# Optimization experiments

Hardware: AMD Instinct MI355X
Metric: run time of the kernel (lower is better)

## Reference

```python
import jax, jax.numpy as jnp
import numpy as np

B, N, T, C = 2, 2048, 32, 32
NUM_BASES, MAX_K, K_CURR = 4, 32, 16


def setup_inputs() -> dict:
    key = jax.random.key(0)
    k1, k2, k3, k4, k5 = jax.random.split(key, 5)
    z = jax.random.normal(k1, (B, N, T, C), dtype=jnp.float32)
    neighbor_indices = jax.random.randint(k2, (N, K_CURR), 0, N)
    # parameters (match torch init scales)
    adjacency = 0.5 + 0.01 * jax.random.normal(k3, (N, MAX_K), dtype=jnp.float32)
    basis_weights = 0.02 * jax.random.normal(k4, (NUM_BASES, N, MAX_K), dtype=jnp.float32)
    channel_coeffs = jax.random.normal(k5, (C, NUM_BASES), dtype=jnp.float32)
    return {
        "z": z,
        "neighbor_indices": neighbor_indices,
        "adjacency": adjacency,
        "basis_weights": basis_weights,
        "channel_coeffs": channel_coeffs,
    }


def reference(z, neighbor_indices, adjacency, basis_weights, channel_coeffs):
    # z: [B,N,T,C], neighbor_indices: [N,k]
    k = neighbor_indices.shape[1]
    bases = basis_weights[:, :, :k]        # [num_bases, N, k]
    adj = adjacency[:, :k]                 # [N, k]
    # per-channel effective edge weights: [C, N, k]
    eff = jnp.einsum('cb,bnk->cnk', channel_coeffs, bases)
    edge_w = eff * adj[None, :, :]         # [C, N, k]
    w = jnp.transpose(edge_w, (1, 2, 0))   # [N, k, C]
    # gather neighbor features: [B, N, k, T, C]
    z_neigh = z[:, neighbor_indices]
    # weighted sum over neighbors, per-channel weights
    out = jnp.einsum('bnktc,nkc->bntc', z_neigh, w)
    return jnp.tanh(out)
```

## Files before the change

### kernel.cpp

```cpp
#include <hip/hip_runtime.h>


constexpr int BB_    = 2;
constexpr int NN_    = 2048;
constexpr int TT_    = 32;
constexpr int CC_    = 32;
constexpr int NBASE_ = 4;
constexpr int MAXK_  = 32;
constexpr int KC_    = 16;

__device__ __forceinline__ float fast_tanh(float x) {
    float e = __expf(2.0f * x);
    float r = __builtin_amdgcn_rcpf(e + 1.0f);
    return fmaf(-2.0f, r, 1.0f);
}

__global__ __launch_bounds__(256) void cgl_kernel(
    const float* __restrict__ z,
    const int*   __restrict__ nbr,
    const float* __restrict__ adj,
    const float* __restrict__ bw,
    const float* __restrict__ cc,
    float*       __restrict__ out)
{
    __shared__ __align__(16) float w_s[KC_][CC_];
    __shared__ float bw_s[NBASE_][KC_];
    __shared__ float cc_s[CC_ * NBASE_];
    __shared__ float adj_s[KC_];
    __shared__ int   idx_s[KC_];

    const int tid = threadIdx.x;
    const int blk = blockIdx.x;
    const int b   = blk >> 11;
    const int n   = blk & (NN_ - 1);

    if (tid < NBASE_ * KC_) {
        int bb = tid >> 4, k = tid & 15;
        bw_s[bb][k] = bw[((size_t)bb * NN_ + n) * MAXK_ + k];
    } else if (tid >= 64 && tid < 64 + CC_ * NBASE_) {
        int i = tid - 64;
        cc_s[i] = cc[i];
    } else if (tid >= 192 && tid < 192 + KC_) {
        int k = tid - 192;
        adj_s[k] = adj[(size_t)n * MAXK_ + k];
        idx_s[k] = nbr[n * KC_ + k];
    }
    __syncthreads();

    {
        int i = tid;
        #pragma unroll
        for (int r = 0; r < 2; ++r, i += 256) {
            int k = i >> 5, c = i & 31;
            float s = cc_s[c * NBASE_ + 0] * bw_s[0][k]
                    + cc_s[c * NBASE_ + 1] * bw_s[1][k]
                    + cc_s[c * NBASE_ + 2] * bw_s[2][k]
                    + cc_s[c * NBASE_ + 3] * bw_s[3][k];
            w_s[k][c] = s * adj_s[k];
        }
    }
    __syncthreads();

    const int c0 = (tid << 2) & 31;
    const float4* __restrict__ z4 = (const float4*)z;
    const size_t zb = (size_t)b * NN_ * (TT_ * CC_ / 4);

    float4 acc = make_float4(0.f, 0.f, 0.f, 0.f);
    #pragma unroll
    for (int k = 0; k < KC_; ++k) {
        const int nk = idx_s[k];
        float4 zv = z4[zb + (size_t)nk * (TT_ * CC_ / 4) + tid];
        float4 wv = *(const float4*)&w_s[k][c0];
        acc.x = fmaf(zv.x, wv.x, acc.x);
        acc.y = fmaf(zv.y, wv.y, acc.y);
        acc.z = fmaf(zv.z, wv.z, acc.z);
        acc.w = fmaf(zv.w, wv.w, acc.w);
    }

    float4 o;
    o.x = fast_tanh(acc.x);
    o.y = fast_tanh(acc.y);
    o.z = fast_tanh(acc.z);
    o.w = fast_tanh(acc.w);
    ((float4*)out)[(size_t)blk * 256 + tid] = o;
}

extern "C" void kernel_launch(void* const* d_in, const int* in_sizes, int n_in,
                              void* d_out, int out_size, void* d_ws, size_t ws_size,
                              hipStream_t stream) {
    const float* z   = (const float*)d_in[0];
    const int*   nbr = (const int*)d_in[1];
    const float* adj = (const float*)d_in[2];
    const float* bw  = (const float*)d_in[3];
    const float* cc  = (const float*)d_in[4];
    float* out = (float*)d_out;

    cgl_kernel<<<dim3(BB_ * NN_), dim3(256), 0, stream>>>(z, nbr, adj, bw, cc, out);
}
```

Measured before the change: 96.64 us.

## Stage z slices in LDS per (b,t,channel-quarter) and precompute bf16 edge weights

Splits the work into a prep kernel that computes the per-channel edge weights once and stores them as packed bf16 in workspace, plus a main kernel that loads a full (batch, time, 8-channel) slice of z for all nodes into LDS. Neighbor gathers then read LDS instead of scattered global memory, and the duplicated per-block weight computation is removed. This adds a second launch and a large shared-memory footprint per block. Rounding the weights to bf16 lowers their precision.

Result: slower. 104.9 us (+8.5%).

```diff
diff --git a/kernel.cpp b/kernel.cpp
--- a/kernel.cpp
+++ b/kernel.cpp
@@ -15,74 +15,114 @@
     return fmaf(-2.0f, r, 1.0f);
 }
 
-__global__ __launch_bounds__(256) void cgl_kernel(
-    const float* __restrict__ z,
-    const int*   __restrict__ nbr,
+__device__ __forceinline__ unsigned pack_bf16(float x, float y) {
+    unsigned ux = __float_as_uint(x), uy = __float_as_uint(y);
+    ux = (ux + 0x7fffu + ((ux >> 16) & 1u)) >> 16;
+    uy = (uy + 0x7fffu + ((uy >> 16) & 1u)) >> 16;
+    return ux | (uy << 16);
+}
+__device__ __forceinline__ float blo(unsigned u) { return __uint_as_float(u << 16); }
+__device__ __forceinline__ float bhi(unsigned u) { return __uint_as_float(u & 0xffff0000u); }
+
+__global__ __launch_bounds__(512) void prep_w(
     const float* __restrict__ adj,
     const float* __restrict__ bw,
     const float* __restrict__ cc,
+    uint4*       __restrict__ w16)
+{
+    const int gid = blockIdx.x * 512 + threadIdx.x;
+    const int n = gid >> 4, k = gid & 15;
+
+    const float a  = adj[n * MAXK_ + k];
+    const float b0 = bw[(0 * NN_ + n) * MAXK_ + k];
+    const float b1 = bw[(1 * NN_ + n) * MAXK_ + k];
+    const float b2 = bw[(2 * NN_ + n) * MAXK_ + k];
+    const float b3 = bw[(3 * NN_ + n) * MAXK_ + k];
+
+    #pragma unroll
+    for (int cq = 0; cq < 4; ++cq) {
+        unsigned u[4];
+        #pragma unroll
+        for (int j = 0; j < 4; ++j) {
+            int c0 = cq * 8 + 2 * j;
+            float w0 = a * (cc[c0 * 4 + 0] * b0 + cc[c0 * 4 + 1] * b1 +
+                            cc[c0 * 4 + 2] * b2 + cc[c0 * 4 + 3] * b3);
+            float w1 = a * (cc[(c0 + 1) * 4 + 0] * b0 + cc[(c0 + 1) * 4 + 1] * b1 +
+                            cc[(c0 + 1) * 4 + 2] * b2 + cc[(c0 + 1) * 4 + 3] * b3);
+            u[j] = pack_bf16(w0, w1);
+        }
+        w16[((size_t)cq * NN_ + n) * KC_ + k] = make_uint4(u[0], u[1], u[2], u[3]);
+    }
+}
+
+__global__ __launch_bounds__(512, 4) void cgl_main(
+    const float* __restrict__ z,
+    const int*   __restrict__ nbr,
+    const uint4* __restrict__ w16,
     float*       __restrict__ out)
 {
-    __shared__ __align__(16) float w_s[KC_][CC_];
-    __shared__ float bw_s[NBASE_][KC_];
-    __shared__ float cc_s[CC_ * NBASE_];
-    __shared__ float adj_s[KC_];
-    __shared__ int   idx_s[KC_];
+    __shared__ float4 zl0[NN_];
+    __shared__ float4 zl1[NN_];
 
-    const int tid = threadIdx.x;
-    const int blk = blockIdx.x;
-    const int b   = blk >> 11;
-    const int n   = blk & (NN_ - 1);
+    const int tid   = threadIdx.x;
+    const int g     = blockIdx.x;
+    const int bt    = g & 63;
+    const int inner = g >> 6;
+    const int cq    = inner >> 1;
+    const int s     = inner & 1;
+    const int b     = bt >> 5;
+    const int t     = bt & 31;
 
-    if (tid < NBASE_ * KC_) {
-        int bb = tid >> 4, k = tid & 15;
-        bw_s[bb][k] = bw[((size_t)bb * NN_ + n) * MAXK_ + k];
-    } else if (tid >= 64 && tid < 64 + CC_ * NBASE_) {
-        int i = tid - 64;
-        cc_s[i] = cc[i];
-    } else if (tid >= 192 && tid < 192 + KC_) {
-        int k = tid - 192;
-        adj_s[k] = adj[(size_t)n * MAXK_ + k];
-        idx_s[k] = nbr[n * KC_ + k];
+    const float* zbase = z + ((size_t)b * NN_ * TT_ + t) * CC_ + cq * 8;
+    #pragma unroll
+    for (int r = 0; r < 4; ++r) {
+        int n = r * 512 + tid;
+        const float4* p = (const float4*)(zbase + (size_t)n * (TT_ * CC_));
+        zl0[n] = p[0];
+        zl1[n] = p[1];
     }
     __syncthreads();
 
-    {
-        int i = tid;
+    #pragma unroll
+    for (int r = 0; r < 2; ++r) {
+        const int n = s * 1024 + r * 512 + tid;
+
+        const int4* ip = (const int4*)(nbr + n * KC_);
+        int4 i0 = ip[0], i1 = ip[1], i2 = ip[2], i3 = ip[3];
+        int idxs[16] = { i0.x, i0.y, i0.z, i0.w,  i1.x, i1.y, i1.z, i1.w,
+                         i2.x, i2.y, i2.z, i2.w,  i3.x, i3.y, i3.z, i3.w };
+
+        const uint4* wp = w16 + ((size_t)cq * NN_ + n) * KC_;
+
+        float acc0 = 0.f, acc1 = 0.f, acc2 = 0.f, acc3 = 0.f;
+        float acc4 = 0.f, acc5 = 0.f, acc6 = 0.f, acc7 = 0.f;
+
         #pragma unroll
-        for (int r = 0; r < 2; ++r, i += 256) {
-            int k = i >> 5, c = i & 31;
-            float s = cc_s[c * NBASE_ + 0] * bw_s[0][k]
-                    + cc_s[c * NBASE_ + 1] * bw_s[1][k]
-                    + cc_s[c * NBASE_ + 2] * bw_s[2][k]
-                    + cc_s[c * NBASE_ + 3] * bw_s[3][k];
-            w_s[k][c] = s * adj_s[k];
+        for (int k = 0; k < KC_; ++k) {
+            const uint4 wv = wp[k];
+            const int nk = idxs[k];
+            const float4 za = zl0[nk];
+            const float4 zb = zl1[nk];
+            acc0 = fmaf(za.x, blo(wv.x), acc0);
+            acc1 = fmaf(za.y, bhi(wv.x), acc1);
+            acc2 = fmaf(za.z, blo(wv.y), acc2);
+            acc3 = fmaf(za.w, bhi(wv.y), acc3);
+            acc4 = fmaf(zb.x, blo(wv.z), acc4);
+            acc5 = fmaf(zb.y, bhi(wv.z), acc5);
+            acc6 = fmaf(zb.z, blo(wv.w), acc6);
+            acc7 = fmaf(zb.w, bhi(wv.w), acc7);
         }
+
+        float4 o0, o1;
+        o0.x = fast_tanh(acc0); o0.y = fast_tanh(acc1);
+        o0.z = fast_tanh(acc2); o0.w = fast_tanh(acc3);
+        o1.x = fast_tanh(acc4); o1.y = fast_tanh(acc5);
+        o1.z = fast_tanh(acc6); o1.w = fast_tanh(acc7);
+
+        float* op = out + ((size_t)(b * NN_ + n) * TT_ + t) * CC_ + cq * 8;
+        ((float4*)op)[0] = o0;
+        ((float4*)op)[1] = o1;
     }
-    __syncthreads();
-
-    const int c0 = (tid << 2) & 31;
-    const float4* __restrict__ z4 = (const float4*)z;
-    const size_t zb = (size_t)b * NN_ * (TT_ * CC_ / 4);
-
-    float4 acc = make_float4(0.f, 0.f, 0.f, 0.f);
-    #pragma unroll
-    for (int k = 0; k < KC_; ++k) {
-        const int nk = idx_s[k];
-        float4 zv = z4[zb + (size_t)nk * (TT_ * CC_ / 4) + tid];
-        float4 wv = *(const float4*)&w_s[k][c0];
-        acc.x = fmaf(zv.x, wv.x, acc.x);
-        acc.y = fmaf(zv.y, wv.y, acc.y);
-        acc.z = fmaf(zv.z, wv.z, acc.z);
-        acc.w = fmaf(zv.w, wv.w, acc.w);
-    }
-
-    float4 o;
-    o.x = fast_tanh(acc.x);
-    o.y = fast_tanh(acc.y);
-    o.z = fast_tanh(acc.z);
-    o.w = fast_tanh(acc.w);
-    ((float4*)out)[(size_t)blk * 256 + tid] = o;
 }
 
 extern "C" void kernel_launch(void* const* d_in, const int* in_sizes, int n_in,
@@ -93,7 +133,9 @@
     const float* adj = (const float*)d_in[2];
     const float* bw  = (const float*)d_in[3];
     const float* cc  = (const float*)d_in[4];
-    float* out = (float*)d_out;
+    float* out  = (float*)d_out;
+    uint4* w16  = (uint4*)d_ws;
 
-    cgl_kernel<<<dim3(BB_ * NN_), dim3(256), 0, stream>>>(z, nbr, adj, bw, cc, out);
+    prep_w<<<dim3(NN_ * KC_ / 512), dim3(512), 0, stream>>>(adj, bw, cc, w16);
+    cgl_main<<<dim3(512), dim3(512), 0, stream>>>(z, nbr, w16, out);
 }
```
